# Performance work log

Measured on AMD Instinct MI355X. Metric: run time of the kernel, lower is better.

## Reference

```python
import jax, jax.numpy as jnp
import numpy as np

D_IN, D_H, D_E, D_MSG, L = 16, 128, 16, 64, 6
N_NODES, N_EDGES, N_GRAPHS = 50000, 1000000, 256
EPS = 1e-5
silu = jax.nn.silu


def _lin(k, fi, fo, shape=None):
    s = shape if shape is not None else (fi, fo)
    return jax.random.normal(k, s, jnp.float32) / np.sqrt(fi)


def setup_inputs() -> dict:
    key = jax.random.key(0)
    ks = iter(jax.random.split(key, 64))
    d = {}
    d['node_feats'] = jax.random.normal(next(ks), (N_NODES, D_IN), jnp.float32)
    d['coords'] = jax.random.normal(next(ks), (N_NODES, 3), jnp.float32)
    d['edge_index'] = jax.random.randint(next(ks), (2, N_EDGES), 0, N_NODES)
    d['edge_feats'] = jax.random.normal(next(ks), (N_EDGES, D_E), jnp.float32)
    d['batch_idx'] = jnp.sort(jax.random.randint(next(ks), (N_NODES,), 0, N_GRAPHS))
    # encoder
    d['enc_w1'] = _lin(next(ks), D_IN, D_H); d['enc_b1'] = jnp.zeros((D_H,), jnp.float32)
    d['enc_w2'] = _lin(next(ks), D_H, D_H); d['enc_b2'] = jnp.zeros((D_H,), jnp.float32)
    # per-layer params, stacked with leading L
    d_msg_in = 2 * D_H + 1 + D_E
    d['pe_w1'] = _lin(next(ks), d_msg_in, D_MSG, (L, d_msg_in, D_MSG)); d['pe_b1'] = jnp.zeros((L, D_MSG), jnp.float32)
    d['pe_w2'] = _lin(next(ks), D_MSG, D_MSG, (L, D_MSG, D_MSG)); d['pe_b2'] = jnp.zeros((L, D_MSG), jnp.float32)
    d['ph_w1'] = _lin(next(ks), D_H + D_MSG, D_H, (L, D_H + D_MSG, D_H)); d['ph_b1'] = jnp.zeros((L, D_H), jnp.float32)
    d['ph_w2'] = _lin(next(ks), D_H, D_H, (L, D_H, D_H)); d['ph_b2'] = jnp.zeros((L, D_H), jnp.float32)
    d['px_w1'] = _lin(next(ks), D_MSG, D_MSG, (L, D_MSG, D_MSG)); d['px_b1'] = jnp.zeros((L, D_MSG), jnp.float32)
    d['px_w2'] = _lin(next(ks), D_MSG, 1, (L, D_MSG, 1)); d['px_b2'] = jnp.zeros((L, 1), jnp.float32)
    d['ln_g'] = jnp.ones((L, D_H), jnp.float32); d['ln_b'] = jnp.zeros((L, D_H), jnp.float32)
    # readout (dropout is inference-mode identity)
    d['ro_w1'] = _lin(next(ks), D_H, D_H); d['ro_b1'] = jnp.zeros((D_H,), jnp.float32)
    d['ro_w2'] = _lin(next(ks), D_H, D_H // 2); d['ro_b2'] = jnp.zeros((D_H // 2,), jnp.float32)
    d['ro_w3'] = _lin(next(ks), D_H // 2, 2); d['ro_b3'] = jnp.zeros((2,), jnp.float32)
    return d


def _layer_norm(x, g, b):
    mu = x.mean(-1, keepdims=True)
    var = ((x - mu) ** 2).mean(-1, keepdims=True)
    return (x - mu) * jax.lax.rsqrt(var + EPS) * g + b


def _egnn_forward(node_feats, coords, edge_index, edge_feats, batch_idx,
                  enc_w1, enc_b1, enc_w2, enc_b2,
                  pe_w1, pe_b1, pe_w2, pe_b2, ph_w1, ph_b1, ph_w2, ph_b2,
                  px_w1, px_b1, px_w2, px_b2, ln_g, ln_b,
                  ro_w1, ro_b1, ro_w2, ro_b2, ro_w3, ro_b3):
    src, dst = edge_index[0], edge_index[1]
    n = node_feats.shape[0]
    h = silu(node_feats @ enc_w1 + enc_b1) @ enc_w2 + enc_b2
    x = coords
    ones_e = jnp.ones((src.shape[0], 1), h.dtype)

    def step(carry, p):
        h, x = carry
        (w1, b1, w2, b2, hw1, hb1, hw2, hb2, xw1, xb1, xw2, xb2, g, b) = p
        diff = x[src] - x[dst]                                   # [E,3]
        sq = (diff ** 2).sum(-1, keepdims=True)                  # [E,1]
        mi = jnp.concatenate([h[src], h[dst], sq, edge_feats], -1)
        msg = silu(silu(mi @ w1 + b1) @ w2 + b2)                 # [E,d_msg]
        count = jnp.maximum(jax.ops.segment_sum(ones_e, dst, num_segments=n), 1.0)
        agg = jax.ops.segment_sum(msg, dst, num_segments=n) / count
        dh = silu(jnp.concatenate([h, agg], -1) @ hw1 + hb1) @ hw2 + hb2
        h_new = _layer_norm(h + dh, g, b)
        w = silu(msg @ xw1 + xb1) @ xw2 + xb2                    # [E,1]
        coord_upd = jax.ops.segment_sum(diff * w, src, num_segments=n) / count
        return (h_new, x + coord_upd), None

    params = (pe_w1, pe_b1, pe_w2, pe_b2, ph_w1, ph_b1, ph_w2, ph_b2,
              px_w1, px_b1, px_w2, px_b2, ln_g, ln_b)
    (h, x), _ = jax.lax.scan(step, (h, x), params)

    gcount = jnp.maximum(jax.ops.segment_sum(jnp.ones((n, 1), h.dtype), batch_idx, num_segments=N_GRAPHS), 1.0)
    graph_h = jax.ops.segment_sum(h, batch_idx, num_segments=N_GRAPHS) / gcount
    r = silu(graph_h @ ro_w1 + ro_b1)
    r = silu(r @ ro_w2 + ro_b2)
    return r @ ro_w3 + ro_b3


def reference(node_feats, coords, edge_index, edge_feats, batch_idx,
              enc_w1, enc_b1, enc_w2, enc_b2,
              pe_w1, pe_b1, pe_w2, pe_b2, ph_w1, ph_b1, ph_w2, ph_b2,
              px_w1, px_b1, px_w2, px_b2, ln_g, ln_b,
              ro_w1, ro_b1, ro_w2, ro_b2, ro_w3, ro_b3):
    return _egnn_forward(node_feats, coords, edge_index, edge_feats, batch_idx,
                         enc_w1, enc_b1, enc_w2, enc_b2,
                         pe_w1, pe_b1, pe_w2, pe_b2, ph_w1, ph_b1, ph_w2, ph_b2,
                         px_w1, px_b1, px_w2, px_b2, ln_g, ln_b,
                         ro_w1, ro_b1, ro_w2, ro_b2, ro_w3, ro_b3)
```

## Files before the change

### kernel.cpp

```cpp
#include <hip/hip_runtime.h>
#include <hip/hip_bf16.h>

#define NN 50000
#define NE 1000000
#define NG 256
#define NL 6
#define NB_SCAN 196
#define EB 128
#define TSTR 66

typedef float v2f __attribute__((ext_vector_type(2)));
typedef short short8 __attribute__((ext_vector_type(8)));
typedef float f32x4 __attribute__((ext_vector_type(4)));

#define MFMA_BF16(a,b,c) __builtin_amdgcn_mfma_f32_16x16x32_bf16(a,b,c,0,0,0)

__device__ __forceinline__ float siluf(float v){
  return v * __builtin_amdgcn_rcpf(1.0f + __expf(-v));
}

__device__ __forceinline__ unsigned f2bf(float x){
  unsigned u = __float_as_uint(x);
  return (u + 0x7FFFu + ((u>>16)&1u)) >> 16;
}
__device__ __forceinline__ float bf2f(unsigned h){
  return __uint_as_float(h<<16);
}

__global__ void k_degrees(const int* __restrict__ ei, int* __restrict__ cnt_dst,
                          int* __restrict__ cnt_src){
  int e = blockIdx.x*256 + threadIdx.x;
  if (e<NE){
    atomicAdd(&cnt_dst[ei[NE+e]], 1);
    atomicAdd(&cnt_src[ei[e]], 1);
  }
}

__global__ void k_scan1(const int* __restrict__ cnt, int* __restrict__ roff,
                        int* __restrict__ bsum){
  __shared__ int sd[256];
  int t=threadIdx.x; int i=blockIdx.x*256+t;
  int v=(i<NN)?cnt[i]:0;
  sd[t]=v; __syncthreads();
  #pragma unroll
  for(int off=1;off<256;off<<=1){
    int xv=(t>=off)?sd[t-off]:0; __syncthreads();
    sd[t]+=xv; __syncthreads();
  }
  if(i<NN) roff[i]=sd[t]-v;
  if(t==255) bsum[blockIdx.x]=sd[t];
}
__global__ void k_scan2(const int* __restrict__ bsum, int* __restrict__ bbase,
                        int* __restrict__ roff){
  __shared__ int sd[256];
  int t=threadIdx.x;
  int v=(t<NB_SCAN)?bsum[t]:0;
  sd[t]=v; __syncthreads();
  #pragma unroll
  for(int off=1;off<256;off<<=1){
    int xv=(t>=off)?sd[t-off]:0; __syncthreads();
    sd[t]+=xv; __syncthreads();
  }
  if(t<NB_SCAN) bbase[t]=sd[t]-v;
  if(t==255) roff[NN]=sd[t];
}
__global__ void k_scan3(int* __restrict__ roff, const int* __restrict__ bbase){
  int i=blockIdx.x*256+threadIdx.x;
  if(i<NN) roff[i]+=bbase[blockIdx.x];
}

__global__ void k_fill(const int* __restrict__ ei,
                       const int* __restrict__ roff_dst, const int* __restrict__ roff_src,
                       int* __restrict__ cur_dst, int* __restrict__ cur_src,
                       int* __restrict__ dlist, int* __restrict__ slist){
  int e = blockIdx.x*256 + threadIdx.x;
  if (e<NE){
    int d = ei[NE+e];
    int pd = roff_dst[d] + atomicAdd(&cur_dst[d],1);
    dlist[pd] = e;
    int s = ei[e];
    int ps = roff_src[s] + atomicAdd(&cur_src[s],1);
    slist[ps] = pd;
  }
}

__global__ void k_gather(const int* __restrict__ ei, const float* __restrict__ ef,
                         const int* __restrict__ dlist,
                         int2* __restrict__ sd_s, unsigned short* __restrict__ efb){
  int p = blockIdx.x*256 + threadIdx.x;
  if (p<NE){
    int e = dlist[p];
    sd_s[p] = make_int2(ei[e], ei[NE+e]);
    int tile = p>>4, l15 = p&15;
    size_t hb = (size_t)tile*512 + (size_t)l15*8;
    const float4* src = (const float4*)(ef + (size_t)e*16);
    #pragma unroll
    for(int q=0;q<4;q++){
      float4 v = src[q];
      float vv[4] = {v.x, v.y, v.z, v.w};
      #pragma unroll
      for(int r=0;r<4;r++){
        int k = q*4+r;
        unsigned h  = f2bf(vv[r]);
        unsigned lo = f2bf(vv[r]-bf2f(h));
        size_t o = hb + (size_t)(k>>3)*128 + (k&7);
        efb[o]     = (unsigned short)h;
        efb[o+256] = (unsigned short)lo;
      }
    }
  }
}

__global__ void k_prep(const float* __restrict__ coords,
                       const int* __restrict__ cnt,
                       float* __restrict__ x, float* __restrict__ cntinv){
  int n = blockIdx.x*256+threadIdx.x;
  if (n<NN){
    x[n*3+0]=coords[n*3+0];
    x[n*3+1]=coords[n*3+1];
    x[n*3+2]=coords[n*3+2];
    cntinv[n]=1.0f/fmaxf((float)cnt[n],1.0f);
  }
}

__global__ void k_wprep(const float* __restrict__ w1full, const float* __restrict__ w2,
                        const float* __restrict__ xw1,
                        unsigned short* __restrict__ blob){
  int t = blockIdx.x*256 + threadIdx.x;
  if (t >= NL*40*64) return;
  int lane = t & 63;
  int f = (t>>6) % 40;
  int l = t / (40*64);
  int m, hl;
  unsigned short* out = blob + (size_t)t*8;
  if (f < 8){
    int mt = f>>1; hl = f&1;
    m = mt*16 + (lane&15);
    int kb = (lane>>4)*8;
    #pragma unroll
    for(int j=0;j<8;j++){
      int k = kb + j;
      float v = (k<16) ? w1full[(size_t)l*273*64 + (size_t)(257+k)*64 + m] : 0.f;
      unsigned h = f2bf(v);
      if (hl) h = f2bf(v - bf2f(h));
      out[j] = (unsigned short)h;
    }
  } else {
    int fi = (f<24) ? (f-8) : (f-24);
    const float* W = ((f<24) ? w2 : xw1) + (size_t)l*4096;
    int mt = fi>>2, kt = (fi>>1)&1; hl = fi&1;
    m = mt*16 + (lane&15);
    int kb = kt*32 + (lane>>4)*8;
    #pragma unroll
    for(int j=0;j<8;j++){
      float v = W[(size_t)(kb+j)*64 + m];
      unsigned h = f2bf(v);
      if (hl) h = f2bf(v - bf2f(h));
      out[j] = (unsigned short)h;
    }
  }
}

__global__ void k_wprep2(const float* __restrict__ pw1, const float* __restrict__ hw1,
                         const float* __restrict__ hw2, unsigned short* __restrict__ blob){
  int t = blockIdx.x*256 + threadIdx.x;
  if (t >= NL*224*64) return;
  int lane = t & 63;
  int f = (t>>6) % 224;
  int l = t / (224*64);
  int m15 = lane & 15, kq = (lane>>4)*8;
  unsigned short* out = blob + (size_t)t*8;
  if (f < 64){
    int mt = f>>3, kt = (f>>1)&3, hl = f&1;
    int m = mt*16 + m15;
    const float* W = pw1 + (size_t)l*273*64;
    #pragma unroll
    for(int j=0;j<8;j++){
      int k = kt*32 + kq + j;
      float v = (m<64) ? W[(size_t)k*64 + m] : W[(size_t)(128+k)*64 + (m-64)];
      unsigned hb = f2bf(v);
      if (hl) hb = f2bf(v - bf2f(hb));
      out[j] = (unsigned short)hb;
    }
  } else if (f < 160){
    int fi = f - 64;
    int mt = fi/12, r = fi%12, kt = r>>1, hl = r&1;
    int m = mt*16 + m15;
    const float* W = hw1 + (size_t)l*192*128;
    #pragma unroll
    for(int j=0;j<8;j++){
      int k = kt*32 + kq + j;
      float v = W[(size_t)k*128 + m];
      unsigned hb = f2bf(v);
      if (hl) hb = f2bf(v - bf2f(hb));
      out[j] = (unsigned short)hb;
    }
  } else {
    int fi = f - 160;
    int mt = fi>>3, kt = (fi>>1)&3, hl = fi&1;
    int m = mt*16 + m15;
    const float* W = hw2 + (size_t)l*128*128;
    #pragma unroll
    for(int j=0;j<8;j++){
      int k = kt*32 + kq + j;
      float v = W[(size_t)k*128 + m];
      unsigned hb = f2bf(v);
      if (hl) hb = f2bf(v - bf2f(hb));
      out[j] = (unsigned short)hb;
    }
  }
}

__global__ void __launch_bounds__(256)
k_encoder(const float* __restrict__ nf,
          const float* __restrict__ w1, const float* __restrict__ b1,
          const float* __restrict__ w2, const float* __restrict__ b2,
          float* __restrict__ h){
  __shared__ float in1[32][17];
  __shared__ float t1[32][129];
  __shared__ float wt[16][136];
  int tid=threadIdx.x;
  int g0=blockIdx.x*32;
  int ty=tid>>4, tx=tid&15;
  int n0=ty*2, n1=ty*2+1;
  { int n=tid>>3, c=(tid&7)*2;
    int gn=g0+n; if(gn>=NN) gn=NN-1;
    float2 v=*(const float2*)(nf+(size_t)gn*16+c);
    in1[n][c]=v.x; in1[n][c+1]=v.y; }
  { int c=tx*8;
    const float* src=w1+(size_t)ty*128+c;
    *(float4*)&wt[ty][c]  =*(const float4*)src;
    *(float4*)&wt[ty][c+4]=*(const float4*)(src+4); }
  __syncthreads();
  float4 a00,a01,a10,a11;
  a00=*(const float4*)(b1+tx*8); a01=*(const float4*)(b1+tx*8+4);
  a10=a00; a11=a01;
  #pragma unroll
  for(int k=0;k<16;k++){
    float m0=in1[n0][k], m1=in1[n1][k];
    float4 wa=*(float4*)&wt[k][tx*8], wb=*(float4*)&wt[k][tx*8+4];
    a00.x+=m0*wa.x; a00.y+=m0*wa.y; a00.z+=m0*wa.z; a00.w+=m0*wa.w;
    a01.x+=m0*wb.x; a01.y+=m0*wb.y; a01.z+=m0*wb.z; a01.w+=m0*wb.w;
    a10.x+=m1*wa.x; a10.y+=m1*wa.y; a10.z+=m1*wa.z; a10.w+=m1*wa.w;
    a11.x+=m1*wb.x; a11.y+=m1*wb.y; a11.z+=m1*wb.z; a11.w+=m1*wb.w;
  }
  int c8=tx*8;
  t1[n0][c8+0]=siluf(a00.x); t1[n0][c8+1]=siluf(a00.y); t1[n0][c8+2]=siluf(a00.z); t1[n0][c8+3]=siluf(a00.w);
  t1[n0][c8+4]=siluf(a01.x); t1[n0][c8+5]=siluf(a01.y); t1[n0][c8+6]=siluf(a01.z); t1[n0][c8+7]=siluf(a01.w);
  t1[n1][c8+0]=siluf(a10.x); t1[n1][c8+1]=siluf(a10.y); t1[n1][c8+2]=siluf(a10.z); t1[n1][c8+3]=siluf(a10.w);
  t1[n1][c8+4]=siluf(a11.x); t1[n1][c8+5]=siluf(a11.y); t1[n1][c8+6]=siluf(a11.z); t1[n1][c8+7]=siluf(a11.w);
  __syncthreads();
  a00=*(const float4*)(b2+c8); a01=*(const float4*)(b2+c8+4);
  a10=a00; a11=a01;
  for(int kt=0;kt<8;kt++){
    { const float* src=w2+(size_t)(kt*16+ty)*128+c8;
      *(float4*)&wt[ty][c8]  =*(const float4*)src;
      *(float4*)&wt[ty][c8+4]=*(const float4*)(src+4); }
    __syncthreads();
    #pragma unroll
    for(int kk=0;kk<16;kk++){
      int k=kt*16+kk;
      float m0=t1[n0][k], m1=t1[n1][k];
      float4 wa=*(float4*)&wt[kk][c8], wb=*(float4*)&wt[kk][c8+4];
      a00.x+=m0*wa.x; a00.y+=m0*wa.y; a00.z+=m0*wa.z; a00.w+=m0*wa.w;
      a01.x+=m0*wb.x; a01.y+=m0*wb.y; a01.z+=m0*wb.z; a01.w+=m0*wb.w;
      a10.x+=m1*wa.x; a10.y+=m1*wa.y; a10.z+=m1*wa.z; a10.w+=m1*wa.w;
      a11.x+=m1*wb.x; a11.y+=m1*wb.y; a11.z+=m1*wb.z; a11.w+=m1*wb.w;
    }
    __syncthreads();
  }
  int gn0=g0+n0, gn1=g0+n1;
  if(gn0<NN){ *(float4*)(h+(size_t)gn0*128+c8)=a00; *(float4*)(h+(size_t)gn0*128+c8+4)=a01; }
  if(gn1<NN){ *(float4*)(h+(size_t)gn1*128+c8)=a10; *(float4*)(h+(size_t)gn1*128+c8+4)=a11; }
}

__device__ __forceinline__ short8 ldB(const unsigned short* base, int row, int kbase){
  const unsigned short* tp = base + row*TSTR + kbase;
  union { unsigned int u[4]; short8 s; } r;
  r.u[0] = *(const unsigned int*)(tp);
  r.u[1] = *(const unsigned int*)(tp+2);
  r.u[2] = *(const unsigned int*)(tp+4);
  r.u[3] = *(const unsigned int*)(tp+6);
  return r.s;
}
__device__ __forceinline__ short8 ldBs(const unsigned short* base, int row, int kbase, int stride){
  const unsigned short* tp = base + row*stride + kbase;
  union { unsigned int u[4]; short8 s; } r;
  r.u[0] = *(const unsigned int*)(tp);
  r.u[1] = *(const unsigned int*)(tp+2);
  r.u[2] = *(const unsigned int*)(tp+4);
  r.u[3] = *(const unsigned int*)(tp+6);
  return r.s;
}

__global__ void __launch_bounds__(256)
k_preM(const float* __restrict__ h, const float* __restrict__ b1,
       const unsigned short* __restrict__ blob,
       float* __restrict__ pa, float* __restrict__ pb){
  __shared__ unsigned short cHi[32*130], cLo[32*130];
  int tid=threadIdx.x;
  int g0=blockIdx.x*32;
  { int n=tid>>3, c0=(tid&7)*16;
    int gn=g0+n; if(gn>=NN) gn=NN-1;
    const float* src=h+(size_t)gn*128+c0;
    #pragma unroll
    for(int q=0;q<4;q++){
      float4 v=*(const float4*)(src+q*4);
      float vv[4]={v.x,v.y,v.z,v.w};
      #pragma unroll
      for(int r=0;r<4;r++){
        unsigned hb=f2bf(vv[r]);
        cHi[n*130+c0+q*4+r]=(unsigned short)hb;
        cLo[n*130+c0+q*4+r]=(unsigned short)f2bf(vv[r]-bf2f(hb));
      }
    } }
  __syncthreads();
  int wl=tid>>6, lane=tid&63, q4=lane>>4, l15=lane&15;
  const short8* fr = (const short8*)blob;
  #pragma unroll
  for(int mi=0;mi<2;mi++){
    int mt = wl + mi*4;
    short8 A[4][2];
    #pragma unroll
    for(int kt=0;kt<4;kt++){
      A[kt][0]=fr[(size_t)((mt*4+kt)*2+0)*64+lane];
      A[kt][1]=fr[(size_t)((mt*4+kt)*2+1)*64+lane];
    }
    f32x4 acc0={0.f,0.f,0.f,0.f}, acc1=acc0;
    #pragma unroll
    for(int kt=0;kt<4;kt++){
      short8 bh0=ldBs(cHi, l15,    kt*32+q4*8, 130);
      short8 bl0=ldBs(cLo, l15,    kt*32+q4*8, 130);
      short8 bh1=ldBs(cHi, 16+l15, kt*32+q4*8, 130);
      short8 bl1=ldBs(cLo, 16+l15, kt*32+q4*8, 130);
      acc0=MFMA_BF16(A[kt][0],bh0,acc0); acc0=MFMA_BF16(A[kt][0],bl0,acc0); acc0=MFMA_BF16(A[kt][1],bh0,acc0);
      acc1=MFMA_BF16(A[kt][0],bh1,acc1); acc1=MFMA_BF16(A[kt][0],bl1,acc1); acc1=MFMA_BF16(A[kt][1],bh1,acc1);
    }
    int m0=mt*16+q4*4;
    float4 bias = (mt<4) ? *(const float4*)(b1+m0) : make_float4(0,0,0,0);
    #pragma unroll
    for(int nt=0;nt<2;nt++){
      f32x4 c = nt ? acc1 : acc0;
      int node=g0+nt*16+l15;
      if(node<NN){
        float4 o = make_float4(c[0]+bias.x, c[1]+bias.y, c[2]+bias.z, c[3]+bias.w);
        if (mt<4) *(float4*)(pa+(size_t)node*64+m0)=o;
        else      *(float4*)(pb+(size_t)node*64+(m0-64))=o;
      }
    }
  }
}

__global__ void __launch_bounds__(512,4)
k_edge2(const int2* __restrict__ sd, const unsigned short* __restrict__ efb,
        const float* __restrict__ x,
        const float* __restrict__ pa, const float* __restrict__ pb,
        const int* __restrict__ roff_dst,
        const float* __restrict__ w1,
        const float* __restrict__ b2,
        const float* __restrict__ xb1,
        const float* __restrict__ xw2, const float* __restrict__ xb2,
        const unsigned short* __restrict__ wblob,
        float* __restrict__ agg, float* __restrict__ wvs){
  __shared__ unsigned short tHi[128*TSTR];
  __shared__ unsigned short tLo[128*TSTR];
  __shared__ unsigned short wlds[40*512];
  __shared__ float sqb[128];
  __shared__ int   sbuf[128], dbuf[128];
  int bid = blockIdx.x;
  int nb = (bid&7)*((int)gridDim.x>>3) + (bid>>3);
  int p0 = nb*EB;
  if (p0 >= NE) return;
  int tid = threadIdx.x;
  int wl = tid>>6, lane = tid&63;
  int q4 = lane>>4, l15 = lane&15;

  float4 st0,st1,st2,st3,st4;
  { const float4* wsrc = (const float4*)wblob;
    st0=wsrc[tid]; st1=wsrc[tid+512]; st2=wsrc[tid+1024]; st3=wsrc[tid+1536]; st4=wsrc[tid+2048]; }

  int tile = nb*8 + wl;
  short8 ebh = {0,0,0,0,0,0,0,0};
  short8 ebl = ebh;
  if (lane < 32){
    const short8* ep = (const short8*)efb + (size_t)tile*64;
    ebh = ep[lane]; ebl = ep[lane+32];
  }

  if (tid < 128){
    int p = p0 + tid;
    int2 sdp = (p<NE) ? sd[p] : make_int2(0,0);
    float sq = 0.f;
    if (p<NE){
      float dx = x[sdp.x*3+0]-x[sdp.y*3+0];
      float dy = x[sdp.x*3+1]-x[sdp.y*3+1];
      float dz = x[sdp.x*3+2]-x[sdp.y*3+2];
      sq = dx*dx+dy*dy+dz*dz;
    }
    sbuf[tid]=sdp.x; dbuf[tid]=sdp.y; sqb[tid]=sq;
  }
  { float4* wd = (float4*)wlds;
    wd[tid]=st0; wd[tid+512]=st1; wd[tid+1024]=st2; wd[tid+1536]=st3; wd[tid+2048]=st4; }
  __syncthreads();

  int rowb = 16*wl + l15;
  int s = sbuf[rowb], d = dbuf[rowb];
  float sqv = sqb[rowb];
  const short8* wfr = (const short8*)wlds;

  #pragma unroll
  for(int mt=0;mt<4;mt++){
    short8 ah = wfr[(2*mt+0)*64+lane];
    short8 al = wfr[(2*mt+1)*64+lane];
    f32x4 c = {0.f,0.f,0.f,0.f};
    c = MFMA_BF16(ah, ebh, c);
    c = MFMA_BF16(ah, ebl, c);
    c = MFMA_BF16(al, ebh, c);
    float4 Ai = *(const float4*)(pa + (size_t)s*64 + mt*16 + q4*4);
    float4 Bi = *(const float4*)(pb + (size_t)d*64 + mt*16 + q4*4);
    float4 Wq = *(const float4*)(w1 + 256*64 + mt*16 + q4*4);
    float v0 = siluf(c[0] + Ai.x + Bi.x + sqv*Wq.x);
    float v1 = siluf(c[1] + Ai.y + Bi.y + sqv*Wq.y);
    float v2 = siluf(c[2] + Ai.z + Bi.z + sqv*Wq.z);
    float v3 = siluf(c[3] + Ai.w + Bi.w + sqv*Wq.w);
    unsigned h0=f2bf(v0),h1=f2bf(v1),h2=f2bf(v2),h3=f2bf(v3);
    unsigned g0=f2bf(v0-bf2f(h0)),g1=f2bf(v1-bf2f(h1)),g2=f2bf(v2-bf2f(h2)),g3=f2bf(v3-bf2f(h3));
    int mo = rowb*TSTR + mt*16 + q4*4;
    *(unsigned*)&tHi[mo]   = h0|(h1<<16);
    *(unsigned*)&tHi[mo+2] = h2|(h3<<16);
    *(unsigned*)&tLo[mo]   = g0|(g1<<16);
    *(unsigned*)&tLo[mo+2] = g2|(g3<<16);
  }

  { short8 bh0 = ldB(tHi, rowb, q4*8);
    short8 bh1 = ldB(tHi, rowb, 32 + q4*8);
    short8 bl0 = ldB(tLo, rowb, q4*8);
    short8 bl1 = ldB(tLo, rowb, 32 + q4*8);
    #pragma unroll
    for(int mt=0;mt<4;mt++){
      short8 ah0 = wfr[(8+mt*4+0)*64+lane];
      short8 al0 = wfr[(8+mt*4+1)*64+lane];
      short8 ah1 = wfr[(8+mt*4+2)*64+lane];
      short8 al1 = wfr[(8+mt*4+3)*64+lane];
      f32x4 c = {0.f,0.f,0.f,0.f};
      c = MFMA_BF16(ah0,bh0,c); c = MFMA_BF16(ah0,bl0,c); c = MFMA_BF16(al0,bh0,c);
      c = MFMA_BF16(ah1,bh1,c); c = MFMA_BF16(ah1,bl1,c); c = MFMA_BF16(al1,bh1,c);
      float4 bb = *(const float4*)(b2 + mt*16 + q4*4);
      float v0=siluf(c[0]+bb.x), v1=siluf(c[1]+bb.y), v2=siluf(c[2]+bb.z), v3=siluf(c[3]+bb.w);
      unsigned h0=f2bf(v0),h1=f2bf(v1),h2=f2bf(v2),h3=f2bf(v3);
      unsigned g0=f2bf(v0-bf2f(h0)),g1=f2bf(v1-bf2f(h1)),g2=f2bf(v2-bf2f(h2)),g3=f2bf(v3-bf2f(h3));
      int mo = rowb*TSTR + mt*16 + q4*4;
      *(unsigned*)&tHi[mo]   = h0|(h1<<16);
      *(unsigned*)&tHi[mo+2] = h2|(h3<<16);
      *(unsigned*)&tLo[mo]   = g0|(g1<<16);
      *(unsigned*)&tLo[mo+2] = g2|(g3<<16);
    } }

  { short8 mh0 = ldB(tHi, rowb, q4*8);
    short8 mh1 = ldB(tHi, rowb, 32 + q4*8);
    short8 ml0 = ldB(tLo, rowb, q4*8);
    short8 ml1 = ldB(tLo, rowb, 32 + q4*8);
    float part = 0.f;
    #pragma unroll
    for(int mt=0;mt<4;mt++){
      short8 ah0 = wfr[(24+mt*4+0)*64+lane];
      short8 al0 = wfr[(24+mt*4+1)*64+lane];
      short8 ah1 = wfr[(24+mt*4+2)*64+lane];
      short8 al1 = wfr[(24+mt*4+3)*64+lane];
      f32x4 c = {0.f,0.f,0.f,0.f};
      c = MFMA_BF16(ah0,mh0,c); c = MFMA_BF16(ah0,ml0,c); c = MFMA_BF16(al0,mh0,c);
      c = MFMA_BF16(ah1,mh1,c); c = MFMA_BF16(ah1,ml1,c); c = MFMA_BF16(al1,mh1,c);
      float4 xb  = *(const float4*)(xb1 + mt*16 + q4*4);
      float4 wv4 = *(const float4*)(xw2 + mt*16 + q4*4);
      part += siluf(c[0]+xb.x)*wv4.x + siluf(c[1]+xb.y)*wv4.y
            + siluf(c[2]+xb.z)*wv4.z + siluf(c[3]+xb.w)*wv4.w;
    }
    part += __shfl_xor(part,16);
    part += __shfl_xor(part,32);
    int pw = p0 + rowb;
    if (q4==0 && pw < NE) wvs[pw] = part + xb2[0];
  }
  __syncthreads();

  int pend = (p0+EB < NE) ? (p0+EB) : NE;
  int dfirst = sd[p0].y;
  int dlast  = sd[pend-1].y;
  int jj = tid&63, slot = tid>>6;
  for (int n=dfirst+slot; n<=dlast; n+=8){
    int rs0 = roff_dst[n], re0 = roff_dst[n+1];
    int rs = (rs0 > p0)   ? rs0 : p0;
    int re = (re0 < pend) ? re0 : pend;
    rs -= p0; re -= p0;
    if (re > rs){
      float sum=0.f;
      for (int r=rs; r<re; r++)
        sum += bf2f((unsigned)tHi[r*TSTR+jj]) + bf2f((unsigned)tLo[r*TSTR+jj]);
      if (rs0 >= p0 && re0 <= pend) agg[(size_t)n*64+jj] = sum;
      else                          atomicAdd(&agg[(size_t)n*64+jj], sum);
    }
  }
}

__global__ void k_coordC(const int2* __restrict__ sd,
                         const int* __restrict__ roff_src, const int* __restrict__ slist,
                         const float* __restrict__ wvs, const float* __restrict__ x,
                         float* __restrict__ cacc){
  int tid=threadIdx.x;
  int grp=tid>>4, sub=tid&15;
  int n = blockIdx.x*16 + grp;
  if (n >= NN) return;
  int s = roff_src[n], e2 = roff_src[n+1];
  float xs0=x[n*3+0], xs1=x[n*3+1], xs2=x[n*3+2];
  float a0=0.f, a1=0.f, a2=0.f;
  for (int p=s+sub; p<e2; p+=16){
    int q = slist[p];
    float w = wvs[q];
    int d = sd[q].y;
    a0 += (xs0 - x[d*3+0])*w;
    a1 += (xs1 - x[d*3+1])*w;
    a2 += (xs2 - x[d*3+2])*w;
  }
  #pragma unroll
  for(int off=1; off<16; off<<=1){
    a0 += __shfl_xor(a0, off);
    a1 += __shfl_xor(a1, off);
    a2 += __shfl_xor(a2, off);
  }
  if (sub==0){
    cacc[n*3+0]=a0; cacc[n*3+1]=a1; cacc[n*3+2]=a2;
  }
}

__global__ void __launch_bounds__(256)
k_nodeM(const float* __restrict__ agg, const float* __restrict__ cacc,
        const float* __restrict__ cntinv,
        const float* __restrict__ hb1, const float* __restrict__ hb2,
        const float* __restrict__ lng, const float* __restrict__ lnb,
        const unsigned short* __restrict__ nbase,
        float* __restrict__ h, float* __restrict__ x){
  __shared__ float hsf[32][129];
  __shared__ unsigned short cHi[32*194], cLo[32*194];
  __shared__ unsigned short t2Hi[32*130], t2Lo[32*130];
  __shared__ float psA[32][8], psB[32][8];
  __shared__ float mu_s[32], rs_s[32];
  int tid=threadIdx.x;
  int g0=blockIdx.x*32;
  { int n=tid>>3, c0=(tid&7)*16;
    int gn=g0+n; if(gn>=NN) gn=NN-1;
    const float* src=h+(size_t)gn*128+c0;
    #pragma unroll
    for(int q=0;q<4;q++){
      float4 v=*(const float4*)(src+q*4);
      float vv[4]={v.x,v.y,v.z,v.w};
      #pragma unroll
      for(int r=0;r<4;r++){
        float val=vv[r];
        hsf[n][c0+q*4+r]=val;
        unsigned hb=f2bf(val);
        cHi[n*194+c0+q*4+r]=(unsigned short)hb;
        cLo[n*194+c0+q*4+r]=(unsigned short)f2bf(val-bf2f(hb));
      }
    }
    float ci=cntinv[gn];
    int ca=(tid&7)*8;
    const float* srca=agg+(size_t)gn*64+ca;
    #pragma unroll
    for(int q=0;q<2;q++){
      float4 v=*(const float4*)(srca+q*4);
      float vv[4]={v.x*ci,v.y*ci,v.z*ci,v.w*ci};
      #pragma unroll
      for(int r=0;r<4;r++){
        unsigned hb=f2bf(vv[r]);
        cHi[n*194+128+ca+q*4+r]=(unsigned short)hb;
        cLo[n*194+128+ca+q*4+r]=(unsigned short)f2bf(vv[r]-bf2f(hb));
      }
    } }
  __syncthreads();
  int wl=tid>>6, lane=tid&63, q4=lane>>4, l15=lane&15;
  const short8* f1 = (const short8*)(nbase + 32768);
  const short8* f2 = (const short8*)(nbase + 81920);
  #pragma unroll
  for(int mi=0;mi<2;mi++){
    int mt=wl+mi*4;
    short8 A[6][2];
    #pragma unroll
    for(int kt=0;kt<6;kt++){
      A[kt][0]=f1[(size_t)((mt*6+kt)*2+0)*64+lane];
      A[kt][1]=f1[(size_t)((mt*6+kt)*2+1)*64+lane];
    }
    f32x4 acc0={0.f,0.f,0.f,0.f}, acc1=acc0;
    #pragma unroll
    for(int kt=0;kt<6;kt++){
      short8 bh0=ldBs(cHi, l15,    kt*32+q4*8, 194);
      short8 bl0=ldBs(cLo, l15,    kt*32+q4*8, 194);
      short8 bh1=ldBs(cHi, 16+l15, kt*32+q4*8, 194);
      short8 bl1=ldBs(cLo, 16+l15, kt*32+q4*8, 194);
      acc0=MFMA_BF16(A[kt][0],bh0,acc0); acc0=MFMA_BF16(A[kt][0],bl0,acc0); acc0=MFMA_BF16(A[kt][1],bh0,acc0);
      acc1=MFMA_BF16(A[kt][0],bh1,acc1); acc1=MFMA_BF16(A[kt][0],bl1,acc1); acc1=MFMA_BF16(A[kt][1],bh1,acc1);
    }
    int m0=mt*16+q4*4;
    float4 bias=*(const float4*)(hb1+m0);
    #pragma unroll
    for(int nt=0;nt<2;nt++){
      f32x4 c = nt ? acc1 : acc0;
      int row=nt*16+l15;
      float v0=siluf(c[0]+bias.x), v1=siluf(c[1]+bias.y), v2=siluf(c[2]+bias.z), v3=siluf(c[3]+bias.w);
      unsigned h0=f2bf(v0),h1=f2bf(v1),h2=f2bf(v2),h3=f2bf(v3);
      unsigned g0b=f2bf(v0-bf2f(h0)),g1b=f2bf(v1-bf2f(h1)),g2b=f2bf(v2-bf2f(h2)),g3b=f2bf(v3-bf2f(h3));
      int mo=row*130+m0;
      *(unsigned*)&t2Hi[mo]  =h0|(h1<<16);  *(unsigned*)&t2Hi[mo+2]=h2|(h3<<16);
      *(unsigned*)&t2Lo[mo]  =g0b|(g1b<<16); *(unsigned*)&t2Lo[mo+2]=g2b|(g3b<<16);
    }
  }
  __syncthreads();
  #pragma unroll
  for(int mi=0;mi<2;mi++){
    int mt=wl+mi*4;
    short8 A[4][2];
    #pragma unroll
    for(int kt=0;kt<4;kt++){
      A[kt][0]=f2[(size_t)((mt*4+kt)*2+0)*64+lane];
      A[kt][1]=f2[(size_t)((mt*4+kt)*2+1)*64+lane];
    }
    f32x4 acc0={0.f,0.f,0.f,0.f}, acc1=acc0;
    #pragma unroll
    for(int kt=0;kt<4;kt++){
      short8 bh0=ldBs(t2Hi, l15,    kt*32+q4*8, 130);
      short8 bl0=ldBs(t2Lo, l15,    kt*32+q4*8, 130);
      short8 bh1=ldBs(t2Hi, 16+l15, kt*32+q4*8, 130);
      short8 bl1=ldBs(t2Lo, 16+l15, kt*32+q4*8, 130);
      acc0=MFMA_BF16(A[kt][0],bh0,acc0); acc0=MFMA_BF16(A[kt][0],bl0,acc0); acc0=MFMA_BF16(A[kt][1],bh0,acc0);
      acc1=MFMA_BF16(A[kt][0],bh1,acc1); acc1=MFMA_BF16(A[kt][0],bl1,acc1); acc1=MFMA_BF16(A[kt][1],bh1,acc1);
    }
    int m0=mt*16+q4*4;
    float4 bias=*(const float4*)(hb2+m0);
    #pragma unroll
    for(int nt=0;nt<2;nt++){
      f32x4 c = nt ? acc1 : acc0;
      int row=nt*16+l15;
      hsf[row][m0+0]+=c[0]+bias.x;
      hsf[row][m0+1]+=c[1]+bias.y;
      hsf[row][m0+2]+=c[2]+bias.z;
      hsf[row][m0+3]+=c[3]+bias.w;
    }
  }
  __syncthreads();
  { int rid=tid>>3, sub=tid&7;
    float sm=0.f, ss=0.f;
    #pragma unroll
    for(int i=0;i<16;i++){ float v=hsf[rid][sub*16+i]; sm+=v; ss+=v*v; }
    psA[rid][sub]=sm; psB[rid][sub]=ss; }
  __syncthreads();
  { int rid=tid>>3, sub=tid&7;
    if(sub==0){
      float sm=0.f, ss=0.f;
      #pragma unroll
      for(int i=0;i<8;i++){ sm+=psA[rid][i]; ss+=psB[rid][i]; }
      float mu=sm*(1.0f/128.0f);
      float var=ss*(1.0f/128.0f)-mu*mu;
      mu_s[rid]=mu; rs_s[rid]=rsqrtf(fmaxf(var,0.0f)+1e-5f);
    } }
  __syncthreads();
  { int rid=tid>>3, sub=tid&7;
    int gn=g0+rid;
    if(gn<NN){
      float mu=mu_s[rid], rs=rs_s[rid];
      int c0=sub*16;
      #pragma unroll
      for(int q=0;q<4;q++){
        float4 g4=*(const float4*)(lng+c0+q*4);
        float4 b4=*(const float4*)(lnb+c0+q*4);
        float4 o;
        o.x=(hsf[rid][c0+q*4+0]-mu)*rs*g4.x+b4.x;
        o.y=(hsf[rid][c0+q*4+1]-mu)*rs*g4.y+b4.y;
        o.z=(hsf[rid][c0+q*4+2]-mu)*rs*g4.z+b4.z;
        o.w=(hsf[rid][c0+q*4+3]-mu)*rs*g4.w+b4.w;
        *(float4*)(h+(size_t)gn*128+c0+q*4)=o;
      }
    } }
  if(tid<32){
    int gn=g0+tid;
    if(gn<NN){
      float ci=cntinv[gn];
      x[gn*3+0]+=cacc[gn*3+0]*ci;
      x[gn*3+1]+=cacc[gn*3+1]*ci;
      x[gn*3+2]+=cacc[gn*3+2]*ci;
    }
  }
}

__device__ __forceinline__ int lowerb(const int* a, int n, int v){
  int lo=0, hi=n;
  while(lo<hi){ int mid=(lo+hi)>>1; if(a[mid]<v) lo=mid+1; else hi=mid; }
  return lo;
}

__global__ void k_readout(const int* __restrict__ batch, const float* __restrict__ h,
                          const float* __restrict__ w1, const float* __restrict__ b1,
                          const float* __restrict__ w2, const float* __restrict__ b2,
                          const float* __restrict__ w3, const float* __restrict__ b3,
                          float* __restrict__ out){
  int g = blockIdx.x;
  int wl = threadIdx.x>>6, lane = threadIdx.x&63;
  __shared__ float part[4][128];
  __shared__ float gh[128];
  __shared__ float r1[128];
  __shared__ float r2[64];
  int start = lowerb(batch, NN, g);
  int end   = lowerb(batch, NN, g+1);
  float s0=0.f, s1=0.f;
  for(int n=start+wl; n<end; n+=4){
    s0 += h[(size_t)n*128+2*lane];
    s1 += h[(size_t)n*128+2*lane+1];
  }
  part[wl][2*lane]=s0; part[wl][2*lane+1]=s1;
  __syncthreads();
  float ci = 1.0f/fmaxf((float)(end-start),1.0f);
  if(wl==0){
    gh[2*lane]   = (part[0][2*lane]+part[1][2*lane]+part[2][2*lane]+part[3][2*lane])*ci;
    gh[2*lane+1] = (part[0][2*lane+1]+part[1][2*lane+1]+part[2][2*lane+1]+part[3][2*lane+1])*ci;
  }
  __syncthreads();
  if(wl==0){
    float a0=b1[2*lane], a1=b1[2*lane+1];
    for(int k=0;k<128;k++){
      float m=gh[k];
      float2 w=((const float2*)(w1+k*128))[lane];
      a0+=m*w.x; a1+=m*w.y;
    }
    r1[2*lane]=siluf(a0); r1[2*lane+1]=siluf(a1);
  }
  __syncthreads();
  if(wl==0){
    float b=b2[lane];
    for(int k=0;k<128;k++) b += r1[k]*w2[k*64+lane];
    r2[lane]=siluf(b);
  }
  __syncthreads();
  if(wl==0 && lane<2){
    float o=b3[lane];
    for(int k=0;k<64;k++) o += r2[k]*w3[k*2+lane];
    out[g*2+lane]=o;
  }
}

extern "C" void kernel_launch(void* const* d_in, const int* in_sizes, int n_in,
                              void* d_out, int out_size, void* d_ws, size_t ws_size,
                              hipStream_t stream){
  const float* nf     = (const float*)d_in[0];
  const float* coords = (const float*)d_in[1];
  const int*   ei     = (const int*)d_in[2];
  const float* ef     = (const float*)d_in[3];
  const int*   batch  = (const int*)d_in[4];

  const float* enc_w1 = (const float*)d_in[5];
  const float* enc_b1 = (const float*)d_in[6];
  const float* enc_w2 = (const float*)d_in[7];
  const float* enc_b2 = (const float*)d_in[8];
  const float* pe_w1  = (const float*)d_in[9];
  const float* pe_b1  = (const float*)d_in[10];
  const float* pe_w2  = (const float*)d_in[11];
  const float* pe_b2  = (const float*)d_in[12];
  const float* ph_w1  = (const float*)d_in[13];
  const float* ph_b1  = (const float*)d_in[14];
  const float* ph_w2  = (const float*)d_in[15];
  const float* ph_b2  = (const float*)d_in[16];
  const float* px_w1  = (const float*)d_in[17];
  const float* px_b1  = (const float*)d_in[18];
  const float* px_w2  = (const float*)d_in[19];
  const float* px_b2  = (const float*)d_in[20];
  const float* ln_g   = (const float*)d_in[21];
  const float* ln_b   = (const float*)d_in[22];
  const float* ro_w1  = (const float*)d_in[23];
  const float* ro_b1  = (const float*)d_in[24];
  const float* ro_w2  = (const float*)d_in[25];
  const float* ro_b2  = (const float*)d_in[26];
  const float* ro_w3  = (const float*)d_in[27];
  const float* ro_b3  = (const float*)d_in[28];

  char* wsb = (char*)d_ws;
  size_t off = 0;
  auto alloc_f = [&](size_t nfl)->float*{ float* p=(float*)(wsb+off); off+=nfl*4; return p; };
  auto alloc_i = [&](size_t nin)->int*  { int*   p=(int*)(wsb+off);   off+=nin*4; return p; };

  float* h      = alloc_f((size_t)NN*128);
  float* x      = alloc_f((size_t)NN*3);
  float* agg    = alloc_f((size_t)NN*64);
  float* cacc   = alloc_f((size_t)NN*3);
  float* cntinv = alloc_f(NN);
  float* pa     = alloc_f((size_t)NN*64);
  float* pb     = alloc_f((size_t)NN*64);
  float* wvs    = alloc_f(NE);
  unsigned short* efb = (unsigned short*)alloc_f((size_t)NE*16 + 2048);
  int2*  sd_s   = (int2*)alloc_i((size_t)NE*2);
  unsigned short* wblob = (unsigned short*)alloc_i((size_t)NL*40*512/2);
  unsigned short* nblob = (unsigned short*)alloc_i((size_t)NL*224*512/2);
  int* roff_dst = alloc_i(NN+1);
  int* roff_src = alloc_i(NN+1);
  int* dlist    = alloc_i(NE);
  int* slist    = alloc_i(NE);
  int* bsum     = alloc_i(256);
  int* bbase    = alloc_i(256);
  int* cnt_dst  = alloc_i(NN);
  int* cnt_src  = alloc_i(NN);
  int* cur_dst  = alloc_i(NN);
  int* cur_src  = alloc_i(NN);

  hipMemsetAsync(cnt_dst, 0, (size_t)4*NN*sizeof(int), stream);
  k_degrees<<<(NE+255)/256,256,0,stream>>>(ei, cnt_dst, cnt_src);
  k_scan1<<<NB_SCAN,256,0,stream>>>(cnt_dst, roff_dst, bsum);
  k_scan2<<<1,256,0,stream>>>(bsum, bbase, roff_dst);
  k_scan3<<<NB_SCAN,256,0,stream>>>(roff_dst, bbase);
  k_scan1<<<NB_SCAN,256,0,stream>>>(cnt_src, roff_src, bsum);
  k_scan2<<<1,256,0,stream>>>(bsum, bbase, roff_src);
  k_scan3<<<NB_SCAN,256,0,stream>>>(roff_src, bbase);
  k_fill<<<(NE+255)/256,256,0,stream>>>(ei, roff_dst, roff_src, cur_dst, cur_src, dlist, slist);
  k_gather<<<(NE+255)/256,256,0,stream>>>(ei, ef, dlist, sd_s, efb);
  k_prep<<<(NN+255)/256,256,0,stream>>>(coords, cnt_dst, x, cntinv);
  k_wprep<<<(NL*40*64+255)/256,256,0,stream>>>(pe_w1, pe_w2, px_w1, wblob);
  k_wprep2<<<(NL*224*64+255)/256,256,0,stream>>>(pe_w1, ph_w1, ph_w2, nblob);
  k_encoder<<<(NN+31)/32,256,0,stream>>>(nf, enc_w1, enc_b1, enc_w2, enc_b2, h);

  int G  = (NE+EB-1)/EB;
  int G8 = ((G+7)/8)*8;

  for(int l=0;l<NL;l++){
    const unsigned short* nbl = nblob + (size_t)l*224*512;
    k_preM<<<(NN+31)/32,256,0,stream>>>(h, pe_b1+l*64, nbl, pa, pb);
    hipMemsetAsync(agg, 0, (size_t)NN*64*sizeof(float), stream);
    k_edge2<<<G8,512,0,stream>>>(sd_s, efb, x, pa, pb, roff_dst,
        pe_w1+(size_t)l*273*64,
        pe_b2+l*64,
        px_b1+l*64,
        px_w2+l*64, px_b2+l,
        wblob + (size_t)l*40*512,
        agg, wvs);
    k_coordC<<<(NN+15)/16,256,0,stream>>>(sd_s, roff_src, slist, wvs, x, cacc);
    k_nodeM<<<(NN+31)/32,256,0,stream>>>(agg, cacc, cntinv,
        ph_b1+l*128, ph_b2+l*128,
        ln_g+l*128, ln_b+l*128, nbl, h, x);
  }

  k_readout<<<NG,256,0,stream>>>(batch, h,
      ro_w1, ro_b1, ro_w2, ro_b2, ro_w3, ro_b3, (float*)d_out);
}
```

Before: 1.889 ms.

## Fuse coordinate scatter into edge kernel with atomics, drop source CSR build

Removes the k_coordC kernel and the whole source-sorted CSR (degree counts, scan, fill). The edge kernel now scatters each edge's coordinate contribution straight into cacc with float atomics on the source node, and the agg memset is widened to also clear cacc. It also replaces per-element bf16 hi/lo splitting with a truncating byte-permute split (split4), and vectorises the segmented agg reduction to two columns per thread. This saves the wvs round-trip and the preprocessing passes, but adds three scattered atomics per edge (about 3M per layer), and both the truncation and the atomic ordering change numerics slightly.

```diff
diff --git a/kernel.cpp b/kernel.cpp
--- a/kernel.cpp
+++ b/kernel.cpp
@@ -27,13 +27,26 @@
   return __uint_as_float(h<<16);
 }
 
-__global__ void k_degrees(const int* __restrict__ ei, int* __restrict__ cnt_dst,
-                          int* __restrict__ cnt_src){
+__device__ __forceinline__ unsigned pkhi(unsigned a, unsigned b){
+  return __builtin_amdgcn_perm(b, a, 0x07060302u);
+}
+__device__ __forceinline__ void split4(float v0,float v1,float v2,float v3,
+                                       unsigned &h01, unsigned &h23,
+                                       unsigned &l01, unsigned &l23){
+  unsigned u0=__float_as_uint(v0),u1=__float_as_uint(v1);
+  unsigned u2=__float_as_uint(v2),u3=__float_as_uint(v3);
+  h01=pkhi(u0,u1); h23=pkhi(u2,u3);
+  float r0=v0-__uint_as_float(u0&0xFFFF0000u);
+  float r1=v1-__uint_as_float(u1&0xFFFF0000u);
+  float r2=v2-__uint_as_float(u2&0xFFFF0000u);
+  float r3=v3-__uint_as_float(u3&0xFFFF0000u);
+  l01=pkhi(__float_as_uint(r0),__float_as_uint(r1));
+  l23=pkhi(__float_as_uint(r2),__float_as_uint(r3));
+}
+
+__global__ void k_degrees(const int* __restrict__ ei, int* __restrict__ cnt_dst){
   int e = blockIdx.x*256 + threadIdx.x;
-  if (e<NE){
-    atomicAdd(&cnt_dst[ei[NE+e]], 1);
-    atomicAdd(&cnt_src[ei[e]], 1);
-  }
+  if (e<NE) atomicAdd(&cnt_dst[ei[NE+e]], 1);
 }
 
 __global__ void k_scan1(const int* __restrict__ cnt, int* __restrict__ roff,
@@ -70,17 +83,13 @@
 }
 
 __global__ void k_fill(const int* __restrict__ ei,
-                       const int* __restrict__ roff_dst, const int* __restrict__ roff_src,
-                       int* __restrict__ cur_dst, int* __restrict__ cur_src,
-                       int* __restrict__ dlist, int* __restrict__ slist){
+                       const int* __restrict__ roff_dst,
+                       int* __restrict__ cur_dst, int* __restrict__ dlist){
   int e = blockIdx.x*256 + threadIdx.x;
   if (e<NE){
     int d = ei[NE+e];
     int pd = roff_dst[d] + atomicAdd(&cur_dst[d],1);
     dlist[pd] = e;
-    int s = ei[e];
-    int ps = roff_src[s] + atomicAdd(&cur_src[s],1);
-    slist[ps] = pd;
   }
 }
 
@@ -306,13 +315,11 @@
     #pragma unroll
     for(int q=0;q<4;q++){
       float4 v=*(const float4*)(src+q*4);
-      float vv[4]={v.x,v.y,v.z,v.w};
-      #pragma unroll
-      for(int r=0;r<4;r++){
-        unsigned hb=f2bf(vv[r]);
-        cHi[n*130+c0+q*4+r]=(unsigned short)hb;
-        cLo[n*130+c0+q*4+r]=(unsigned short)f2bf(vv[r]-bf2f(hb));
-      }
+      unsigned h01,h23,l01,l23;
+      split4(v.x,v.y,v.z,v.w,h01,h23,l01,l23);
+      int o=n*130+c0+q*4;
+      *(unsigned*)&cHi[o]=h01; *(unsigned*)&cHi[o+2]=h23;
+      *(unsigned*)&cLo[o]=l01; *(unsigned*)&cLo[o+2]=l23;
     } }
   __syncthreads();
   int wl=tid>>6, lane=tid&63, q4=lane>>4, l15=lane&15;
@@ -361,11 +368,11 @@
         const float* __restrict__ xb1,
         const float* __restrict__ xw2, const float* __restrict__ xb2,
         const unsigned short* __restrict__ wblob,
-        float* __restrict__ agg, float* __restrict__ wvs){
+        float* __restrict__ agg, float* __restrict__ cacc){
   __shared__ unsigned short tHi[128*TSTR];
   __shared__ unsigned short tLo[128*TSTR];
   __shared__ unsigned short wlds[40*512];
-  __shared__ float sqb[128];
+  __shared__ float sqb[128], dxb[128], dyb[128], dzb[128];
   __shared__ int   sbuf[128], dbuf[128];
   int bid = blockIdx.x;
   int nb = (bid&7)*((int)gridDim.x>>3) + (bid>>3);
@@ -390,14 +397,15 @@
   if (tid < 128){
     int p = p0 + tid;
     int2 sdp = (p<NE) ? sd[p] : make_int2(0,0);
-    float sq = 0.f;
+    float dx=0.f, dy=0.f, dz=0.f;
     if (p<NE){
-      float dx = x[sdp.x*3+0]-x[sdp.y*3+0];
-      float dy = x[sdp.x*3+1]-x[sdp.y*3+1];
-      float dz = x[sdp.x*3+2]-x[sdp.y*3+2];
-      sq = dx*dx+dy*dy+dz*dz;
-    }
-    sbuf[tid]=sdp.x; dbuf[tid]=sdp.y; sqb[tid]=sq;
+      dx = x[sdp.x*3+0]-x[sdp.y*3+0];
+      dy = x[sdp.x*3+1]-x[sdp.y*3+1];
+      dz = x[sdp.x*3+2]-x[sdp.y*3+2];
+    }
+    sbuf[tid]=sdp.x; dbuf[tid]=sdp.y;
+    sqb[tid]=dx*dx+dy*dy+dz*dz;
+    dxb[tid]=dx; dyb[tid]=dy; dzb[tid]=dz;
   }
   { float4* wd = (float4*)wlds;
     wd[tid]=st0; wd[tid+512]=st1; wd[tid+1024]=st2; wd[tid+1536]=st3; wd[tid+2048]=st4; }
@@ -423,13 +431,13 @@
     float v1 = siluf(c[1] + Ai.y + Bi.y + sqv*Wq.y);
     float v2 = siluf(c[2] + Ai.z + Bi.z + sqv*Wq.z);
     float v3 = siluf(c[3] + Ai.w + Bi.w + sqv*Wq.w);
-    unsigned h0=f2bf(v0),h1=f2bf(v1),h2=f2bf(v2),h3=f2bf(v3);
-    unsigned g0=f2bf(v0-bf2f(h0)),g1=f2bf(v1-bf2f(h1)),g2=f2bf(v2-bf2f(h2)),g3=f2bf(v3-bf2f(h3));
+    unsigned h01,h23,l01,l23;
+    split4(v0,v1,v2,v3,h01,h23,l01,l23);
     int mo = rowb*TSTR + mt*16 + q4*4;
-    *(unsigned*)&tHi[mo]   = h0|(h1<<16);
-    *(unsigned*)&tHi[mo+2] = h2|(h3<<16);
-    *(unsigned*)&tLo[mo]   = g0|(g1<<16);
-    *(unsigned*)&tLo[mo+2] = g2|(g3<<16);
+    *(unsigned*)&tHi[mo]   = h01;
+    *(unsigned*)&tHi[mo+2] = h23;
+    *(unsigned*)&tLo[mo]   = l01;
+    *(unsigned*)&tLo[mo+2] = l23;
   }
 
   { short8 bh0 = ldB(tHi, rowb, q4*8);
@@ -447,13 +455,13 @@
       c = MFMA_BF16(ah1,bh1,c); c = MFMA_BF16(ah1,bl1,c); c = MFMA_BF16(al1,bh1,c);
       float4 bb = *(const float4*)(b2 + mt*16 + q4*4);
       float v0=siluf(c[0]+bb.x), v1=siluf(c[1]+bb.y), v2=siluf(c[2]+bb.z), v3=siluf(c[3]+bb.w);
-      unsigned h0=f2bf(v0),h1=f2bf(v1),h2=f2bf(v2),h3=f2bf(v3);
-      unsigned g0=f2bf(v0-bf2f(h0)),g1=f2bf(v1-bf2f(h1)),g2=f2bf(v2-bf2f(h2)),g3=f2bf(v3-bf2f(h3));
+      unsigned h01,h23,l01,l23;
+      split4(v0,v1,v2,v3,h01,h23,l01,l23);
       int mo = rowb*TSTR + mt*16 + q4*4;
-      *(unsigned*)&tHi[mo]   = h0|(h1<<16);
-      *(unsigned*)&tHi[mo+2] = h2|(h3<<16);
-      *(unsigned*)&tLo[mo]   = g0|(g1<<16);
-      *(unsigned*)&tLo[mo+2] = g2|(g3<<16);
+      *(unsigned*)&tHi[mo]   = h01;
+      *(unsigned*)&tHi[mo+2] = h23;
+      *(unsigned*)&tLo[mo]   = l01;
+      *(unsigned*)&tLo[mo+2] = l23;
     } }
 
   { short8 mh0 = ldB(tHi, rowb, q4*8);
@@ -478,56 +486,40 @@
     part += __shfl_xor(part,16);
     part += __shfl_xor(part,32);
     int pw = p0 + rowb;
-    if (q4==0 && pw < NE) wvs[pw] = part + xb2[0];
+    if (q4==0 && pw < NE){
+      float wv = part + xb2[0];
+      atomicAdd(&cacc[3*s+0], dxb[rowb]*wv);
+      atomicAdd(&cacc[3*s+1], dyb[rowb]*wv);
+      atomicAdd(&cacc[3*s+2], dzb[rowb]*wv);
+    }
   }
   __syncthreads();
 
   int pend = (p0+EB < NE) ? (p0+EB) : NE;
   int dfirst = sd[p0].y;
   int dlast  = sd[pend-1].y;
-  int jj = tid&63, slot = tid>>6;
-  for (int n=dfirst+slot; n<=dlast; n+=8){
+  int jj = (tid&31)*2, slot = tid>>5;
+  for (int n=dfirst+slot; n<=dlast; n+=16){
     int rs0 = roff_dst[n], re0 = roff_dst[n+1];
     int rs = (rs0 > p0)   ? rs0 : p0;
     int re = (re0 < pend) ? re0 : pend;
     rs -= p0; re -= p0;
     if (re > rs){
-      float sum=0.f;
-      for (int r=rs; r<re; r++)
-        sum += bf2f((unsigned)tHi[r*TSTR+jj]) + bf2f((unsigned)tLo[r*TSTR+jj]);
-      if (rs0 >= p0 && re0 <= pend) agg[(size_t)n*64+jj] = sum;
-      else                          atomicAdd(&agg[(size_t)n*64+jj], sum);
-    }
-  }
-}
-
-__global__ void k_coordC(const int2* __restrict__ sd,
-                         const int* __restrict__ roff_src, const int* __restrict__ slist,
-                         const float* __restrict__ wvs, const float* __restrict__ x,
-                         float* __restrict__ cacc){
-  int tid=threadIdx.x;
-  int grp=tid>>4, sub=tid&15;
-  int n = blockIdx.x*16 + grp;
-  if (n >= NN) return;
-  int s = roff_src[n], e2 = roff_src[n+1];
-  float xs0=x[n*3+0], xs1=x[n*3+1], xs2=x[n*3+2];
-  float a0=0.f, a1=0.f, a2=0.f;
-  for (int p=s+sub; p<e2; p+=16){
-    int q = slist[p];
-    float w = wvs[q];
-    int d = sd[q].y;
-    a0 += (xs0 - x[d*3+0])*w;
-    a1 += (xs1 - x[d*3+1])*w;
-    a2 += (xs2 - x[d*3+2])*w;
-  }
-  #pragma unroll
-  for(int off=1; off<16; off<<=1){
-    a0 += __shfl_xor(a0, off);
-    a1 += __shfl_xor(a1, off);
-    a2 += __shfl_xor(a2, off);
-  }
-  if (sub==0){
-    cacc[n*3+0]=a0; cacc[n*3+1]=a1; cacc[n*3+2]=a2;
+      float s0=0.f, s1=0.f;
+      for (int r=rs; r<re; r++){
+        unsigned dh = *(const unsigned*)&tHi[r*TSTR+jj];
+        unsigned dl = *(const unsigned*)&tLo[r*TSTR+jj];
+        s0 += __uint_as_float(dh<<16) + __uint_as_float(dl<<16);
+        s1 += __uint_as_float(dh&0xFFFF0000u) + __uint_as_float(dl&0xFFFF0000u);
+      }
+      if (rs0 >= p0 && re0 <= pend){
+        float2 o = make_float2(s0,s1);
+        *(float2*)&agg[(size_t)n*64+jj] = o;
+      } else {
+        atomicAdd(&agg[(size_t)n*64+jj], s0);
+        atomicAdd(&agg[(size_t)n*64+jj+1], s1);
+      }
+    }
   }
 }
 
@@ -538,7 +530,7 @@
         const float* __restrict__ lng, const float* __restrict__ lnb,
         const unsigned short* __restrict__ nbase,
         float* __restrict__ h, float* __restrict__ x){
-  __shared__ float hsf[32][129];
+  __shared__ float hsf[32][132];
   __shared__ unsigned short cHi[32*194], cLo[32*194];
   __shared__ unsigned short t2Hi[32*130], t2Lo[32*130];
   __shared__ float psA[32][8], psB[32][8];
@@ -551,15 +543,12 @@
     #pragma unroll
     for(int q=0;q<4;q++){
       float4 v=*(const float4*)(src+q*4);
-      float vv[4]={v.x,v.y,v.z,v.w};
-      #pragma unroll
-      for(int r=0;r<4;r++){
-        float val=vv[r];
-        hsf[n][c0+q*4+r]=val;
-        unsigned hb=f2bf(val);
-        cHi[n*194+c0+q*4+r]=(unsigned short)hb;
-        cLo[n*194+c0+q*4+r]=(unsigned short)f2bf(val-bf2f(hb));
-      }
+      *(float4*)&hsf[n][c0+q*4]=v;
+      unsigned h01,h23,l01,l23;
+      split4(v.x,v.y,v.z,v.w,h01,h23,l01,l23);
+      int o=n*194+c0+q*4;
+      *(unsigned*)&cHi[o]=h01; *(unsigned*)&cHi[o+2]=h23;
+      *(unsigned*)&cLo[o]=l01; *(unsigned*)&cLo[o+2]=l23;
     }
     float ci=cntinv[gn];
     int ca=(tid&7)*8;
@@ -567,13 +556,11 @@
     #pragma unroll
     for(int q=0;q<2;q++){
       float4 v=*(const float4*)(srca+q*4);
-      float vv[4]={v.x*ci,v.y*ci,v.z*ci,v.w*ci};
-      #pragma unroll
-      for(int r=0;r<4;r++){
-        unsigned hb=f2bf(vv[r]);
-        cHi[n*194+128+ca+q*4+r]=(unsigned short)hb;
-        cLo[n*194+128+ca+q*4+r]=(unsigned short)f2bf(vv[r]-bf2f(hb));
-      }
+      unsigned h01,h23,l01,l23;
+      split4(v.x*ci,v.y*ci,v.z*ci,v.w*ci,h01,h23,l01,l23);
+      int o=n*194+128+ca+q*4;
+      *(unsigned*)&cHi[o]=h01; *(unsigned*)&cHi[o+2]=h23;
+      *(unsigned*)&cLo[o]=l01; *(unsigned*)&cLo[o+2]=l23;
     } }
   __syncthreads();
   int wl=tid>>6, lane=tid&63, q4=lane>>4, l15=lane&15;
@@ -605,11 +592,11 @@
       f32x4 c = nt ? acc1 : acc0;
       int row=nt*16+l15;
       float v0=siluf(c[0]+bias.x), v1=siluf(c[1]+bias.y), v2=siluf(c[2]+bias.z), v3=siluf(c[3]+bias.w);
-      unsigned h0=f2bf(v0),h1=f2bf(v1),h2=f2bf(v2),h3=f2bf(v3);
-      unsigned g0b=f2bf(v0-bf2f(h0)),g1b=f2bf(v1-bf2f(h1)),g2b=f2bf(v2-bf2f(h2)),g3b=f2bf(v3-bf2f(h3));
+      unsigned h01,h23,l01,l23;
+      split4(v0,v1,v2,v3,h01,h23,l01,l23);
       int mo=row*130+m0;
-      *(unsigned*)&t2Hi[mo]  =h0|(h1<<16);  *(unsigned*)&t2Hi[mo+2]=h2|(h3<<16);
-      *(unsigned*)&t2Lo[mo]  =g0b|(g1b<<16); *(unsigned*)&t2Lo[mo+2]=g2b|(g3b<<16);
+      *(unsigned*)&t2Hi[mo]=h01; *(unsigned*)&t2Hi[mo+2]=h23;
+      *(unsigned*)&t2Lo[mo]=l01; *(unsigned*)&t2Lo[mo+2]=l23;
     }
   }
   __syncthreads();
@@ -790,31 +777,23 @@
   float* cntinv = alloc_f(NN);
   float* pa     = alloc_f((size_t)NN*64);
   float* pb     = alloc_f((size_t)NN*64);
-  float* wvs    = alloc_f(NE);
   unsigned short* efb = (unsigned short*)alloc_f((size_t)NE*16 + 2048);
   int2*  sd_s   = (int2*)alloc_i((size_t)NE*2);
   unsigned short* wblob = (unsigned short*)alloc_i((size_t)NL*40*512/2);
   unsigned short* nblob = (unsigned short*)alloc_i((size_t)NL*224*512/2);
   int* roff_dst = alloc_i(NN+1);
-  int* roff_src = alloc_i(NN+1);
   int* dlist    = alloc_i(NE);
-  int* slist    = alloc_i(NE);
   int* bsum     = alloc_i(256);
   int* bbase    = alloc_i(256);
   int* cnt_dst  = alloc_i(NN);
-  int* cnt_src  = alloc_i(NN);
   int* cur_dst  = alloc_i(NN);
-  int* cur_src  = alloc_i(NN);
-
-  hipMemsetAsync(cnt_dst, 0, (size_t)4*NN*sizeof(int), stream);
-  k_degrees<<<(NE+255)/256,256,0,stream>>>(ei, cnt_dst, cnt_src);
+
+  hipMemsetAsync(cnt_dst, 0, (size_t)2*NN*sizeof(int), stream);
+  k_degrees<<<(NE+255)/256,256,0,stream>>>(ei, cnt_dst);
   k_scan1<<<NB_SCAN,256,0,stream>>>(cnt_dst, roff_dst, bsum);
   k_scan2<<<1,256,0,stream>>>(bsum, bbase, roff_dst);
   k_scan3<<<NB_SCAN,256,0,stream>>>(roff_dst, bbase);
-  k_scan1<<<NB_SCAN,256,0,stream>>>(cnt_src, roff_src, bsum);
-  k_scan2<<<1,256,0,stream>>>(bsum, bbase, roff_src);
-  k_scan3<<<NB_SCAN,256,0,stream>>>(roff_src, bbase);
-  k_fill<<<(NE+255)/256,256,0,stream>>>(ei, roff_dst, roff_src, cur_dst, cur_src, dlist, slist);
+  k_fill<<<(NE+255)/256,256,0,stream>>>(ei, roff_dst, cur_dst, dlist);
   k_gather<<<(NE+255)/256,256,0,stream>>>(ei, ef, dlist, sd_s, efb);
   k_prep<<<(NN+255)/256,256,0,stream>>>(coords, cnt_dst, x, cntinv);
   k_wprep<<<(NL*40*64+255)/256,256,0,stream>>>(pe_w1, pe_w2, px_w1, wblob);
@@ -827,15 +806,14 @@
   for(int l=0;l<NL;l++){
     const unsigned short* nbl = nblob + (size_t)l*224*512;
     k_preM<<<(NN+31)/32,256,0,stream>>>(h, pe_b1+l*64, nbl, pa, pb);
-    hipMemsetAsync(agg, 0, (size_t)NN*64*sizeof(float), stream);
+    hipMemsetAsync(agg, 0, (size_t)NN*67*sizeof(float), stream);
     k_edge2<<<G8,512,0,stream>>>(sd_s, efb, x, pa, pb, roff_dst,
         pe_w1+(size_t)l*273*64,
         pe_b2+l*64,
         px_b1+l*64,
         px_w2+l*64, px_b2+l,
         wblob + (size_t)l*40*512,
-        agg, wvs);
-    k_coordC<<<(NN+15)/16,256,0,stream>>>(sd_s, roff_src, slist, wvs, x, cacc);
+        agg, cacc);
     k_nodeM<<<(NN+31)/32,256,0,stream>>>(agg, cacc, cntinv,
         ph_b1+l*128, ph_b2+l*128,
         ln_g+l*128, ln_b+l*128, nbl, h, x);
```

Measured after the change: 1.902 ms. No clear change (+0.7%).
